# Performance work log

Measured on AMD Instinct MI355X. Metric: run time of the kernel, lower is better.

The kernel has to match this reference:

```python
import jax, jax.numpy as jnp
import numpy as np

B, H, W, N, DX, DZ = 4, 64, 64, 4096, 2, 128
INIT_LS = 0.1


def setup_inputs() -> dict:
    key = jax.random.key(0)
    k1, k2, k3, k4 = jax.random.split(key, 4)
    xc_off_grid = jax.random.uniform(k1, (B, N, DX), dtype=jnp.float32)
    # regular grid coordinates in [0, 1]^2, broadcast over batch
    gy, gx = jnp.meshgrid(jnp.linspace(0.0, 1.0, H), jnp.linspace(0.0, 1.0, W), indexing="ij")
    xc_on_grid = jnp.broadcast_to(jnp.stack([gy, gx], axis=-1)[None], (B, H, W, DX)).astype(jnp.float32)
    zc_off_grid = jax.random.normal(k2, (B, N, DZ), dtype=jnp.float32)
    zc_on_grid = jax.random.normal(k3, (B, H, W, DZ), dtype=jnp.float32)
    # lengthscale_param = log(exp(init_lengthscale) - 1)  (inverse softplus)
    lengthscale_param = jnp.log(jnp.expm1(jnp.full((DX,), INIT_LS, dtype=jnp.float32)))
    return {
        "xc_off_grid": xc_off_grid,
        "xc_on_grid": xc_on_grid,
        "zc_off_grid": zc_off_grid,
        "zc_on_grid": zc_on_grid,
        "lengthscale_param": lengthscale_param,
        "ignore_on_grid": 0,
    }


def reference(xc_off_grid, xc_on_grid, zc_off_grid, zc_on_grid, lengthscale_param, ignore_on_grid):
    b = xc_on_grid.shape[0]
    grid_shape = xc_on_grid.shape[1:-1]
    dz = zc_off_grid.shape[-1]
    xg = xc_on_grid.reshape(b, -1, xc_on_grid.shape[-1])  # [b, m, dx]
    lengthscale = 1e-05 + jax.nn.softplus(lengthscale_param)  # [dx]
    # squared scaled distances: [b, m, n]
    diff = (xg[:, :, None, :] - xc_off_grid[:, None, :, :]) / lengthscale
    weights = jnp.exp(-0.5 * jnp.sum(diff * diff, axis=-1))  # [b, m, n]
    zc = jnp.einsum("bmn,bnd->bmd", weights, zc_off_grid)  # [b, m, dz]
    if not ignore_on_grid:
        zc = zc + zc_on_grid.reshape(b, -1, dz)
    return zc.reshape((b,) + grid_shape + (dz,))
```

## Files before the change

### kernel.cpp

```cpp
#include <hip/hip_runtime.h>

#define HH 64
#define WW 64
#define NN 4096
#define DZc 128
#define KS 8
#define BK 32
#define NKT (NN / KS / BK)
#define CELLS 2097152
#define WS_NEED (8ull * CELLS * 2ull)

typedef __fp16 v2fp16 __attribute__((ext_vector_type(2)));
typedef _Float16 v4h __attribute__((ext_vector_type(4)));
typedef _Float16 v8h __attribute__((ext_vector_type(8)));
typedef float v16f __attribute__((ext_vector_type(16)));

__device__ __forceinline__ unsigned pk16(float lo, float hi){
  union { v2fp16 h; unsigned u; } c;
  c.h = __builtin_amdgcn_cvt_pkrtz(lo, hi);
  return c.u;
}
__device__ __forceinline__ float fexp2(float x){ return __builtin_amdgcn_exp2f(x); }

__global__ void init_out_kernel(const float4* __restrict__ zc_on,
                                const int* __restrict__ ignore,
                                float4* __restrict__ out){
  int i = blockIdx.x * blockDim.x + threadIdx.x;
  float4 v = zc_on[i];
  if (ignore[0]) { v.x = 0.f; v.y = 0.f; v.z = 0.f; v.w = 0.f; }
  out[i] = v;
}

__global__ void reduce_kernel(const v4h* __restrict__ part,
                              const float4* __restrict__ zc_on,
                              const int* __restrict__ ignore,
                              float4* __restrict__ out){
  int i = blockIdx.x * blockDim.x + threadIdx.x;
  float4 s = zc_on[i];
  if (ignore[0]) { s.x = 0.f; s.y = 0.f; s.z = 0.f; s.w = 0.f; }
  #pragma unroll
  for (int ks = 0; ks < KS; ++ks){
    v4h p = part[(size_t)ks * (CELLS / 4) + i];
    s.x += (float)p[0]; s.y += (float)p[1]; s.z += (float)p[2]; s.w += (float)p[3];
  }
  out[i] = s;
}

__global__ __launch_bounds__(256, 4)
void setconv_gemm_kernel(const float* __restrict__ xc_off,
                         const float* __restrict__ xc_on,
                         const float* __restrict__ zc_off,
                         const float* __restrict__ lsp,
                         _Float16* __restrict__ part,
                         float* __restrict__ out)
{
  __shared__ unsigned short zt[2][128][34];
  __shared__ unsigned short gt[2][24][48];

  const int tid = threadIdx.x;
  const int bid = blockIdx.x;
  const int ks  = bid >> 7;
  const int rem = bid & 127;
  const int b   = rem >> 5;
  const int mt  = rem & 31;
  const int iy0 = (mt >> 3) * 16;
  const int ix0 = (mt & 7) * 8;
  const int nbase = ks * (NN / KS);

  const float lsy = 1e-5f + log1pf(expf(lsp[0]));
  const float lsx = 1e-5f + log1pf(expf(lsp[1]));
  const float LOG2E = 1.44269504088896340736f;
  const float ay = -0.5f * LOG2E / (lsy * lsy);
  const float ax = -0.5f * LOG2E / (lsx * lsx);

  const int gp = tid & 15;
  const int grow = tid >> 4;
  const float gcy = xc_on[((b * HH + iy0 + grow) * WW) * 2];
  const bool hasx = (tid < 128);
  const float gcx = hasx ? xc_on[(b * HH * WW + ix0 + grow) * 2 + 1] : 0.f;

  const int zd = tid & 127;
  const int nh = tid >> 7;

  const int lane = tid & 63;
  const int wv  = tid >> 6;
  const int wm  = wv >> 1;
  const int wdh = wv & 1;
  const int l31 = lane & 31;
  const int lh  = lane >> 5;
  const int gxr = 16 + (l31 & 7);
  const int gyr = wm * 8 + (l31 >> 3);

  v16f acc[2][2];
  #pragma unroll
  for (int m = 0; m < 2; ++m)
    #pragma unroll
    for (int d = 0; d < 2; ++d)
      #pragma unroll
      for (int r = 0; r < 16; ++r)
        acc[m][d][r] = 0.f;

  const float* xb = xc_off + (size_t)b * NN * 2;
  const float* zb = zc_off + (size_t)b * NN * DZc;

  {
    const int n0 = nbase;
    float4 xq = *(const float4*)&xb[(size_t)(n0 + 2 * gp) * 2];
    float dy0 = gcy - xq.x, dy1 = gcy - xq.z;
    ((unsigned*)&gt[0][0][0])[grow * 24 + gp] = pk16(fexp2(ay * dy0 * dy0), fexp2(ay * dy1 * dy1));
    if (hasx){
      float dx0 = gcx - xq.y, dx1 = gcx - xq.w;
      ((unsigned*)&gt[0][0][0])[(16 + grow) * 24 + gp] = pk16(fexp2(ax * dx0 * dx0), fexp2(ax * dx1 * dx1));
    }
    float zv[16];
    #pragma unroll
    for (int i = 0; i < 16; ++i)
      zv[i] = zb[(size_t)(n0 + nh * 16 + i) * DZc + zd];
    #pragma unroll
    for (int j = 0; j < 4; ++j){
      union { unsigned u[2]; double d; } w;
      w.u[0] = pk16(zv[4 * j],     zv[4 * j + 1]);
      w.u[1] = pk16(zv[4 * j + 2], zv[4 * j + 3]);
      *(double*)&zt[0][zd][nh * 16 + 4 * j] = w.d;
    }
  }
  __syncthreads();

  #pragma unroll 1
  for (int kt = 0; kt < NKT; ++kt){
    const int buf  = kt & 1;
    const int nbuf = buf ^ 1;
    const bool have_next = (kt + 1 < NKT);
    const int n1 = nbase + (kt + 1) * BK;

    float zv[16];
    float4 xq_n = (float4){0.f, 0.f, 0.f, 0.f};
    if (have_next){
      #pragma unroll
      for (int i = 0; i < 16; ++i)
        zv[i] = zb[(size_t)(n1 + nh * 16 + i) * DZc + zd];
      xq_n = *(const float4*)&xb[(size_t)(n1 + 2 * gp) * 2];
    }

    #pragma unroll
    for (int kstep = 0; kstep < 2; ++kstep){
      const int k0 = kstep * 16 + lh * 8;
      const v8h xu = *(const v8h*)&gt[buf][gxr][k0];
      v8h bfr[2];
      #pragma unroll
      for (int dtl = 0; dtl < 2; ++dtl){
        union { v4h h[2]; v8h v; } zu;
        zu.h[0] = *(const v4h*)&zt[buf][wdh * 64 + dtl * 32 + l31][k0];
        zu.h[1] = *(const v4h*)&zt[buf][wdh * 64 + dtl * 32 + l31][k0 + 4];
        bfr[dtl] = zu.v;
      }
      #pragma unroll
      for (int mtl = 0; mtl < 2; ++mtl){
        const v8h yu = *(const v8h*)&gt[buf][gyr + mtl * 4][k0];
        v8h av = yu * xu;
        #pragma unroll
        for (int dtl = 0; dtl < 2; ++dtl)
          acc[mtl][dtl] = __builtin_amdgcn_mfma_f32_32x32x16_f16(av, bfr[dtl], acc[mtl][dtl], 0, 0, 0);
      }
    }

    if (have_next){
      #pragma unroll
      for (int j = 0; j < 4; ++j){
        union { unsigned u[2]; double d; } w;
        w.u[0] = pk16(zv[4 * j],     zv[4 * j + 1]);
        w.u[1] = pk16(zv[4 * j + 2], zv[4 * j + 3]);
        *(double*)&zt[nbuf][zd][nh * 16 + 4 * j] = w.d;
      }
      float dy0 = gcy - xq_n.x, dy1 = gcy - xq_n.z;
      ((unsigned*)&gt[nbuf][0][0])[grow * 24 + gp] = pk16(fexp2(ay * dy0 * dy0), fexp2(ay * dy1 * dy1));
      if (hasx){
        float dx0 = gcx - xq_n.y, dx1 = gcx - xq_n.w;
        ((unsigned*)&gt[nbuf][0][0])[(16 + grow) * 24 + gp] = pk16(fexp2(ax * dx0 * dx0), fexp2(ax * dx1 * dx1));
      }
    }
    __syncthreads();
  }

  if (part){
    _Float16* pw = part + (size_t)ks * CELLS;
    #pragma unroll
    for (int mtl = 0; mtl < 2; ++mtl)
      #pragma unroll
      for (int dtl = 0; dtl < 2; ++dtl){
        const int d = wdh * 64 + dtl * 32 + l31;
        #pragma unroll
        for (int reg = 0; reg < 16; ++reg){
          const int row = (reg & 3) + 8 * (reg >> 2) + 4 * lh;
          const int m = wm * 64 + mtl * 32 + row;
          const int iy = iy0 + (m >> 3);
          const int ix = ix0 + (m & 7);
          pw[((b * HH + iy) * WW + ix) * DZc + d] = (_Float16)acc[mtl][dtl][reg];
        }
      }
  } else {
    #pragma unroll
    for (int mtl = 0; mtl < 2; ++mtl)
      #pragma unroll
      for (int dtl = 0; dtl < 2; ++dtl){
        const int d = wdh * 64 + dtl * 32 + l31;
        #pragma unroll
        for (int reg = 0; reg < 16; ++reg){
          const int row = (reg & 3) + 8 * (reg >> 2) + 4 * lh;
          const int m = wm * 64 + mtl * 32 + row;
          const int iy = iy0 + (m >> 3);
          const int ix = ix0 + (m & 7);
          unsafeAtomicAdd(&out[((b * HH + iy) * WW + ix) * DZc + d], acc[mtl][dtl][reg]);
        }
      }
  }
}

extern "C" void kernel_launch(void* const* d_in, const int* in_sizes, int n_in,
                              void* d_out, int out_size, void* d_ws, size_t ws_size,
                              hipStream_t stream){
  const float* xc_off = (const float*)d_in[0];
  const float* xc_on  = (const float*)d_in[1];
  const float* zc_off = (const float*)d_in[2];
  const float* zc_on  = (const float*)d_in[3];
  const float* lsp    = (const float*)d_in[4];
  const int*   ign    = (const int*)d_in[5];
  float* out = (float*)d_out;

  if (ws_size >= WS_NEED){
    _Float16* part = (_Float16*)d_ws;
    setconv_gemm_kernel<<<KS * 128, 256, 0, stream>>>(xc_off, xc_on, zc_off, lsp, part, out);
    reduce_kernel<<<CELLS / 4 / 256, 256, 0, stream>>>((const v4h*)part, (const float4*)zc_on, ign, (float4*)out);
  } else {
    init_out_kernel<<<out_size / 1024, 256, 0, stream>>>((const float4*)zc_on, ign, (float4*)out);
    setconv_gemm_kernel<<<KS * 128, 256, 0, stream>>>(xc_off, xc_on, zc_off, lsp, nullptr, out);
  }
}
```

Measured before the change: 114.0 us.

## Precompute all Gaussian factors in LDS and feed z operands straight from registers

Each block now computes the separable Gaussian factor table for its whole 512-point K range once into shared memory, up front. The per-iteration barrier and LDS double buffering are gone. The z operand for the MFMA B fragment is loaded directly from global memory into registers in the fragment layout, prefetched one step ahead and packed to fp16 without staging in LDS. This removes the per-tile __syncthreads and the LDS round trip for z. In exchange, each lane issues strided scalar global loads of z, and 16 values in flight per step may expose memory latency.

Result: slower. 116.8 us (+2.4%).

```diff
diff --git a/kernel.cpp b/kernel.cpp
--- a/kernel.cpp
+++ b/kernel.cpp
@@ -5,8 +5,8 @@
 #define NN 4096
 #define DZc 128
 #define KS 8
-#define BK 32
-#define NKT (NN / KS / BK)
+#define KRANGE (NN / KS)
+#define NSTEP (KRANGE / 16)
 #define CELLS 2097152
 #define WS_NEED (8ull * CELLS * 2ull)
 
@@ -54,8 +54,7 @@
                          _Float16* __restrict__ part,
                          float* __restrict__ out)
 {
-  __shared__ unsigned short zt[2][128][34];
-  __shared__ unsigned short gt[2][24][48];
+  __shared__ unsigned short gt[24 * 520];
 
   const int tid = threadIdx.x;
   const int bid = blockIdx.x;
@@ -65,7 +64,7 @@
   const int mt  = rem & 31;
   const int iy0 = (mt >> 3) * 16;
   const int ix0 = (mt & 7) * 8;
-  const int nbase = ks * (NN / KS);
+  const int nbase = ks * KRANGE;
 
   const float lsy = 1e-5f + log1pf(expf(lsp[0]));
   const float lsx = 1e-5f + log1pf(expf(lsp[1]));
@@ -73,14 +72,35 @@
   const float ay = -0.5f * LOG2E / (lsy * lsy);
   const float ax = -0.5f * LOG2E / (lsx * lsx);
 
-  const int gp = tid & 15;
-  const int grow = tid >> 4;
-  const float gcy = xc_on[((b * HH + iy0 + grow) * WW) * 2];
-  const bool hasx = (tid < 128);
-  const float gcx = hasx ? xc_on[(b * HH * WW + ix0 + grow) * 2 + 1] : 0.f;
-
-  const int zd = tid & 127;
-  const int nh = tid >> 7;
+  const float* xb = xc_off + (size_t)b * NN * 2;
+  const float* zb = zc_off + (size_t)b * NN * DZc;
+
+  {
+    const int g  = tid >> 5;
+    const int p8 = tid & 31;
+    float cc[3], aa[3];
+    #pragma unroll
+    for (int rr = 0; rr < 3; ++rr){
+      int r = 3 * g + rr;
+      if (r < 16){ cc[rr] = xc_on[((b * HH + iy0 + r) * WW) * 2];          aa[rr] = ay; }
+      else       { cc[rr] = xc_on[(b * HH * WW + ix0 + (r - 16)) * 2 + 1]; aa[rr] = ax; }
+    }
+    unsigned* gtw = (unsigned*)gt;
+    #pragma unroll
+    for (int j = 0; j < 8; ++j){
+      const int p = p8 + 32 * j;
+      float4 xq = *(const float4*)&xb[(size_t)(nbase + 2 * p) * 2];
+      #pragma unroll
+      for (int rr = 0; rr < 3; ++rr){
+        int r = 3 * g + rr;
+        float s0 = (r < 16) ? xq.x : xq.y;
+        float s1 = (r < 16) ? xq.z : xq.w;
+        float d0 = cc[rr] - s0, d1 = cc[rr] - s1;
+        gtw[r * 260 + p] = pk16(fexp2(aa[rr] * d0 * d0), fexp2(aa[rr] * d1 * d1));
+      }
+    }
+  }
+  __syncthreads();
 
   const int lane = tid & 63;
   const int wv  = tid >> 6;
@@ -88,8 +108,8 @@
   const int wdh = wv & 1;
   const int l31 = lane & 31;
   const int lh  = lane >> 5;
-  const int gxr = 16 + (l31 & 7);
-  const int gyr = wm * 8 + (l31 >> 3);
+  const int gxr  = 16 + (l31 & 7);
+  const int gyr0 = wm * 8 + (l31 >> 3);
 
   v16f acc[2][2];
   #pragma unroll
@@ -100,86 +120,47 @@
       for (int r = 0; r < 16; ++r)
         acc[m][d][r] = 0.f;
 
-  const float* xb = xc_off + (size_t)b * NN * 2;
-  const float* zb = zc_off + (size_t)b * NN * DZc;
-
-  {
-    const int n0 = nbase;
-    float4 xq = *(const float4*)&xb[(size_t)(n0 + 2 * gp) * 2];
-    float dy0 = gcy - xq.x, dy1 = gcy - xq.z;
-    ((unsigned*)&gt[0][0][0])[grow * 24 + gp] = pk16(fexp2(ay * dy0 * dy0), fexp2(ay * dy1 * dy1));
-    if (hasx){
-      float dx0 = gcx - xq.y, dx1 = gcx - xq.w;
-      ((unsigned*)&gt[0][0][0])[(16 + grow) * 24 + gp] = pk16(fexp2(ax * dx0 * dx0), fexp2(ax * dx1 * dx1));
-    }
-    float zv[16];
-    #pragma unroll
-    for (int i = 0; i < 16; ++i)
-      zv[i] = zb[(size_t)(n0 + nh * 16 + i) * DZc + zd];
-    #pragma unroll
-    for (int j = 0; j < 4; ++j){
-      union { unsigned u[2]; double d; } w;
-      w.u[0] = pk16(zv[4 * j],     zv[4 * j + 1]);
-      w.u[1] = pk16(zv[4 * j + 2], zv[4 * j + 3]);
-      *(double*)&zt[0][zd][nh * 16 + 4 * j] = w.d;
-    }
-  }
-  __syncthreads();
+  const float* zp0 = zb + (size_t)(nbase + lh * 8) * DZc + wdh * 64 + l31;
+
+  float pend[16];
+  #pragma unroll
+  for (int dtl = 0; dtl < 2; ++dtl)
+    #pragma unroll
+    for (int j = 0; j < 8; ++j)
+      pend[dtl * 8 + j] = zp0[j * DZc + dtl * 32];
 
   #pragma unroll 1
-  for (int kt = 0; kt < NKT; ++kt){
-    const int buf  = kt & 1;
-    const int nbuf = buf ^ 1;
-    const bool have_next = (kt + 1 < NKT);
-    const int n1 = nbase + (kt + 1) * BK;
-
-    float zv[16];
-    float4 xq_n = (float4){0.f, 0.f, 0.f, 0.f};
-    if (have_next){
-      #pragma unroll
-      for (int i = 0; i < 16; ++i)
-        zv[i] = zb[(size_t)(n1 + nh * 16 + i) * DZc + zd];
-      xq_n = *(const float4*)&xb[(size_t)(n1 + 2 * gp) * 2];
-    }
-
-    #pragma unroll
-    for (int kstep = 0; kstep < 2; ++kstep){
-      const int k0 = kstep * 16 + lh * 8;
-      const v8h xu = *(const v8h*)&gt[buf][gxr][k0];
-      v8h bfr[2];
-      #pragma unroll
-      for (int dtl = 0; dtl < 2; ++dtl){
-        union { v4h h[2]; v8h v; } zu;
-        zu.h[0] = *(const v4h*)&zt[buf][wdh * 64 + dtl * 32 + l31][k0];
-        zu.h[1] = *(const v4h*)&zt[buf][wdh * 64 + dtl * 32 + l31][k0 + 4];
-        bfr[dtl] = zu.v;
-      }
-      #pragma unroll
-      for (int mtl = 0; mtl < 2; ++mtl){
-        const v8h yu = *(const v8h*)&gt[buf][gyr + mtl * 4][k0];
-        v8h av = yu * xu;
+  for (int s = 0; s < NSTEP; ++s){
+    const int k0 = s * 16 + lh * 8;
+
+    v8h bfr[2];
+    #pragma unroll
+    for (int dtl = 0; dtl < 2; ++dtl){
+      union { unsigned u[4]; v8h v; } u;
+      #pragma unroll
+      for (int jj = 0; jj < 4; ++jj)
+        u.u[jj] = pk16(pend[dtl * 8 + 2 * jj], pend[dtl * 8 + 2 * jj + 1]);
+      bfr[dtl] = u.v;
+    }
+
+    if (s + 1 < NSTEP){
+      const float* zp = zp0 + (size_t)(s + 1) * 16 * DZc;
+      #pragma unroll
+      for (int dtl = 0; dtl < 2; ++dtl)
         #pragma unroll
-        for (int dtl = 0; dtl < 2; ++dtl)
-          acc[mtl][dtl] = __builtin_amdgcn_mfma_f32_32x32x16_f16(av, bfr[dtl], acc[mtl][dtl], 0, 0, 0);
-      }
-    }
-
-    if (have_next){
-      #pragma unroll
-      for (int j = 0; j < 4; ++j){
-        union { unsigned u[2]; double d; } w;
-        w.u[0] = pk16(zv[4 * j],     zv[4 * j + 1]);
-        w.u[1] = pk16(zv[4 * j + 2], zv[4 * j + 3]);
-        *(double*)&zt[nbuf][zd][nh * 16 + 4 * j] = w.d;
-      }
-      float dy0 = gcy - xq_n.x, dy1 = gcy - xq_n.z;
-      ((unsigned*)&gt[nbuf][0][0])[grow * 24 + gp] = pk16(fexp2(ay * dy0 * dy0), fexp2(ay * dy1 * dy1));
-      if (hasx){
-        float dx0 = gcx - xq_n.y, dx1 = gcx - xq_n.w;
-        ((unsigned*)&gt[nbuf][0][0])[(16 + grow) * 24 + gp] = pk16(fexp2(ax * dx0 * dx0), fexp2(ax * dx1 * dx1));
-      }
-    }
-    __syncthreads();
+        for (int j = 0; j < 8; ++j)
+          pend[dtl * 8 + j] = zp[j * DZc + dtl * 32];
+    }
+
+    const v8h gx = *(const v8h*)&gt[gxr * 520 + k0];
+    #pragma unroll
+    for (int mtl = 0; mtl < 2; ++mtl){
+      const v8h gy = *(const v8h*)&gt[(gyr0 + mtl * 4) * 520 + k0];
+      v8h av = gy * gx;
+      #pragma unroll
+      for (int dtl = 0; dtl < 2; ++dtl)
+        acc[mtl][dtl] = __builtin_amdgcn_mfma_f32_32x32x16_f16(av, bfr[dtl], acc[mtl][dtl], 0, 0, 0);
+    }
   }
 
   if (part){
```
